# Kernel tuning notes

Measured on AMD Instinct MI355X. Metric: run time of the kernel, lower is better.

## Reference

```python
import jax, jax.numpy as jnp
import numpy as np

R = 65536          # N_rays
S = 128            # samples per ray
N = R * S          # total samples
L_OP = 0.05        # lambda_opacity (module arg)
L_DIST = 0.001     # lambda_distortion (module arg)
C_RGB = 1.0        # config.lambda_rgb
C_OP = 1.0         # config.lambda_opacity
C_EIK = 0.1        # config.lambda_eikonal


def setup_inputs() -> dict:
    key = jax.random.key(0)
    k = jax.random.split(key, 8)
    rgb = jax.random.uniform(k[0], (R, 3), dtype=jnp.float32)
    target_rays = jax.random.uniform(k[1], (R, 3), dtype=jnp.float32)
    opacity = jax.random.uniform(k[2], (R,), dtype=jnp.float32, minval=1e-4, maxval=1.0)
    grad = jax.random.normal(k[3], (N, 3), dtype=jnp.float32)
    ws = jax.random.uniform(k[4], (N,), dtype=jnp.float32) / S
    deltas = jax.random.uniform(k[5], (N,), dtype=jnp.float32) / S
    # midpoints sorted within each ray segment
    ts = jnp.sort(jax.random.uniform(k[6], (R, S), dtype=jnp.float32), axis=1).reshape(N)
    ray_idx = jax.random.permutation(k[7], R).astype(jnp.int32)
    rays_a = jnp.stack([ray_idx,
                        (jnp.arange(R) * S).astype(jnp.int32),
                        jnp.full((R,), S, dtype=jnp.int32)], axis=1)
    return dict(rgb=rgb, target_rays=target_rays, opacity=opacity, grad=grad,
                ws=ws, deltas=deltas, ts=ts, rays_a=rays_a)


def _smooth_l1(x, y):
    d = jnp.abs(x - y)
    return jnp.mean(jnp.where(d < 1.0, 0.5 * d * d, d - 0.5))


def _distortion_loss(ws, deltas, ts, rays_a):
    # Mip-NeRF 360 distortion via per-segment exclusive prefix sums:
    # loss_r = sum_i 2*w_i*(t_i*W_i^< - WT_i^<) + (1/3) sum_i w_i^2 * delta_i
    n = ws.shape[0]
    n_rays = rays_a.shape[0]
    ray_idx = rays_a[:, 0]
    starts = rays_a[:, 1]                      # sorted ascending (contiguous layout)
    pos = jnp.arange(n)
    seg = jnp.searchsorted(starts, pos, side='right') - 1   # row in rays_a per sample
    cw = jnp.cumsum(ws)
    cwt = jnp.cumsum(ws * ts)
    sm1 = jnp.maximum(starts - 1, 0)
    base_w = jnp.where(starts > 0, cw[sm1], 0.0)
    base_wt = jnp.where(starts > 0, cwt[sm1], 0.0)
    excl_w = cw - ws - base_w[seg]             # exclusive scan of w within segment
    excl_wt = cwt - ws * ts - base_wt[seg]     # exclusive scan of w*t within segment
    per = 2.0 * ws * (ts * excl_w - excl_wt) + ws * ws * deltas / 3.0
    per_row = jax.ops.segment_sum(per, seg, num_segments=n_rays)
    # scatter row losses to their ray index -> (N_rays,)
    return jnp.zeros(n_rays, ws.dtype).at[ray_idx].set(per_row)


def reference(rgb, target_rays, opacity, grad, ws, deltas, ts, rays_a):
    d_rgb = _smooth_l1(rgb, target_rays) * C_RGB
    d_op = L_OP * (-opacity * jnp.log(opacity)) * C_OP          # (N_rays,)
    d_eik = jnp.mean((jnp.linalg.norm(grad, axis=-1) - 1.0) ** 2) * C_EIK
    d_dist = L_DIST * _distortion_loss(ws, deltas, ts, rays_a)  # (N_rays,)
    # pack dict values into one flat array: [rgb, opacity(R), eikonal, distortion(R)]
    return jnp.concatenate([d_rgb[None], d_op, d_eik[None], d_dist])
```

## Files before the change

### kernel.cpp

```cpp
#include <hip/hip_runtime.h>
#include <math.h>

#define R_RAYS 65536
#define S_SAMP 128
#define NSLOTS 1024

__global__ void init_ws_kernel(float* __restrict__ w) {
    int i = blockIdx.x * blockDim.x + threadIdx.x;
    if (i < 2 * NSLOTS) w[i] = 0.f;
}

__device__ __forceinline__ float wave_incl_scan(float x, int lane) {
#pragma unroll
    for (int off = 1; off < 64; off <<= 1) {
        float v = __shfl_up(x, off, 64);
        if (lane >= off) x += v;
    }
    return x;
}

__global__ __launch_bounds__(128) void nerf_main_kernel(
    const float* __restrict__ rgb, const float* __restrict__ tgt,
    const float* __restrict__ opacity, const float* __restrict__ grad,
    const float* __restrict__ ws, const float* __restrict__ deltas,
    const float* __restrict__ ts, const int* __restrict__ rays_a,
    float* __restrict__ out, float* __restrict__ partials)
{
    const int r    = blockIdx.x;
    const int tid  = threadIdx.x;
    const int lane = tid & 63;
    const int wave = tid >> 6;

    const int ridx  = rays_a[3 * r + 0];
    const int start = rays_a[3 * r + 1];
    const int i = start + tid;

    const float w = ws[i];
    const float t = ts[i];
    const float d = deltas[i];
    const float wt = w * t;

    float iw  = wave_incl_scan(w, lane);
    float iwt = wave_incl_scan(wt, lane);
    __shared__ float s_w[2], s_wt[2];
    if (lane == 63) { s_w[wave] = iw; s_wt[wave] = iwt; }
    __syncthreads();
    const float bw  = (wave == 1) ? s_w[0]  : 0.f;
    const float bwt = (wave == 1) ? s_wt[0] : 0.f;
    const float ew  = iw  - w  + bw;
    const float ewt = iwt - wt + bwt;

    float per = 2.f * w * (t * ew - ewt) + w * w * d * (1.f / 3.f);

    const float gx = grad[3 * i + 0];
    const float gy = grad[3 * i + 1];
    const float gz = grad[3 * i + 2];
    const float nrm = sqrtf(gx * gx + gy * gy + gz * gz);
    float ek = (nrm - 1.f) * (nrm - 1.f);

#pragma unroll
    for (int off = 32; off > 0; off >>= 1) {
        per += __shfl_down(per, off, 64);
        ek  += __shfl_down(ek,  off, 64);
    }
    __shared__ float s_per[2], s_ek[2];
    if (lane == 0) { s_per[wave] = per; s_ek[wave] = ek; }
    __syncthreads();

    if (tid == 0) {
        out[2 + R_RAYS + ridx] = 0.001f * (s_per[0] + s_per[1]);
    } else if (tid == 1) {
        atomicAdd(&partials[r & (NSLOTS - 1)], s_ek[0] + s_ek[1]);
    } else if (tid == 2) {
        const float op = opacity[r];
        out[1 + r] = 0.05f * (-op * logf(op));
    } else if (tid == 3) {
        float srgb = 0.f;
#pragma unroll
        for (int c = 0; c < 3; ++c) {
            const float diff = fabsf(rgb[3 * r + c] - tgt[3 * r + c]);
            srgb += (diff < 1.f) ? 0.5f * diff * diff : (diff - 0.5f);
        }
        atomicAdd(&partials[NSLOTS + (r & (NSLOTS - 1))], srgb);
    }
}

__global__ __launch_bounds__(1024) void nerf_final_kernel(
    const float* __restrict__ partials, float* __restrict__ out)
{
    const int tid  = threadIdx.x;
    const int lane = tid & 63;
    const int wave = tid >> 6;

    float ek = partials[tid];
    float rg = partials[NSLOTS + tid];
#pragma unroll
    for (int off = 32; off > 0; off >>= 1) {
        ek += __shfl_down(ek, off, 64);
        rg += __shfl_down(rg, off, 64);
    }
    __shared__ float s_ek[16], s_rg[16];
    if (lane == 0) { s_ek[wave] = ek; s_rg[wave] = rg; }
    __syncthreads();
    if (tid == 0) {
        float tek = 0.f, trg = 0.f;
#pragma unroll
        for (int j = 0; j < 16; ++j) { tek += s_ek[j]; trg += s_rg[j]; }
        out[0]          = trg / (3.f * (float)R_RAYS);
        out[1 + R_RAYS] = 0.1f * tek / ((float)R_RAYS * (float)S_SAMP);
    }
}

extern "C" void kernel_launch(void* const* d_in, const int* in_sizes, int n_in,
                              void* d_out, int out_size, void* d_ws, size_t ws_size,
                              hipStream_t stream) {
    const float* rgb     = (const float*)d_in[0];
    const float* tgt     = (const float*)d_in[1];
    const float* opacity = (const float*)d_in[2];
    const float* grad    = (const float*)d_in[3];
    const float* ws      = (const float*)d_in[4];
    const float* deltas  = (const float*)d_in[5];
    const float* ts      = (const float*)d_in[6];
    const int*   rays_a  = (const int*)d_in[7];
    float* out      = (float*)d_out;
    float* partials = (float*)d_ws;

    init_ws_kernel<<<(2 * NSLOTS + 255) / 256, 256, 0, stream>>>(partials);
    nerf_main_kernel<<<R_RAYS, 128, 0, stream>>>(rgb, tgt, opacity, grad, ws,
                                                 deltas, ts, rays_a, out, partials);
    nerf_final_kernel<<<1, 1024, 0, stream>>>(partials, out);
}
```

Baseline: 238.9 us.

## Process 8 rays per block with float4 loads and per-block partials

Restructures the main kernel so each 32-lane group handles one ray with four samples per thread, loaded as float4, and does a thread-local serial scan followed by a 32-wide shuffle scan. The grid shrinks from 65536 blocks to 8192. The atomic accumulation into slots and the init kernel are replaced by deterministic per-block partial sums that the final kernel reduces. This cuts block-launch overhead, the wide scans and atomics, at the cost of more registers per thread and an assumption that segment starts are 16-byte aligned.

After: 230.6 us. 1.04x faster.

```diff
diff --git a/kernel.cpp b/kernel.cpp
--- a/kernel.cpp
+++ b/kernel.cpp
@@ -3,85 +3,103 @@
 
 #define R_RAYS 65536
 #define S_SAMP 128
-#define NSLOTS 1024
+#define RAYS_PER_BLOCK 8
+#define NB (R_RAYS / RAYS_PER_BLOCK)
 
-__global__ void init_ws_kernel(float* __restrict__ w) {
-    int i = blockIdx.x * blockDim.x + threadIdx.x;
-    if (i < 2 * NSLOTS) w[i] = 0.f;
-}
-
-__device__ __forceinline__ float wave_incl_scan(float x, int lane) {
-#pragma unroll
-    for (int off = 1; off < 64; off <<= 1) {
-        float v = __shfl_up(x, off, 64);
-        if (lane >= off) x += v;
-    }
-    return x;
-}
-
-__global__ __launch_bounds__(128) void nerf_main_kernel(
+__global__ __launch_bounds__(256) void nerf_main_kernel(
     const float* __restrict__ rgb, const float* __restrict__ tgt,
     const float* __restrict__ opacity, const float* __restrict__ grad,
     const float* __restrict__ ws, const float* __restrict__ deltas,
     const float* __restrict__ ts, const int* __restrict__ rays_a,
     float* __restrict__ out, float* __restrict__ partials)
 {
-    const int r    = blockIdx.x;
     const int tid  = threadIdx.x;
+    const int wave = tid >> 6;
     const int lane = tid & 63;
-    const int wave = tid >> 6;
+    const int grp  = tid >> 5;
+    const int l32  = tid & 31;
+    const int b    = blockIdx.x;
+    const int r    = b * RAYS_PER_BLOCK + grp;
 
     const int ridx  = rays_a[3 * r + 0];
     const int start = rays_a[3 * r + 1];
-    const int i = start + tid;
+    const int i0    = start + l32 * 4;
 
-    const float w = ws[i];
-    const float t = ts[i];
-    const float d = deltas[i];
-    const float wt = w * t;
+    const float4 w4 = *(const float4*)(ws + i0);
+    const float4 t4 = *(const float4*)(ts + i0);
+    const float4 d4 = *(const float4*)(deltas + i0);
+    const float wv[4] = { w4.x, w4.y, w4.z, w4.w };
+    const float tv[4] = { t4.x, t4.y, t4.z, t4.w };
+    const float dv[4] = { d4.x, d4.y, d4.z, d4.w };
 
-    float iw  = wave_incl_scan(w, lane);
-    float iwt = wave_incl_scan(wt, lane);
-    __shared__ float s_w[2], s_wt[2];
-    if (lane == 63) { s_w[wave] = iw; s_wt[wave] = iwt; }
-    __syncthreads();
-    const float bw  = (wave == 1) ? s_w[0]  : 0.f;
-    const float bwt = (wave == 1) ? s_wt[0] : 0.f;
-    const float ew  = iw  - w  + bw;
-    const float ewt = iwt - wt + bwt;
+    float wtv[4];
+    float sw = 0.f, swt = 0.f;
+#pragma unroll
+    for (int j = 0; j < 4; ++j) { wtv[j] = wv[j] * tv[j]; sw += wv[j]; swt += wtv[j]; }
 
-    float per = 2.f * w * (t * ew - ewt) + w * w * d * (1.f / 3.f);
+    float isw = sw, iswt = swt;
+#pragma unroll
+    for (int off = 1; off < 32; off <<= 1) {
+        const float a = __shfl_up(isw,  off, 32);
+        const float c = __shfl_up(iswt, off, 32);
+        if (l32 >= off) { isw += a; iswt += c; }
+    }
+    float ew  = isw  - sw;
+    float ewt = iswt - swt;
 
-    const float gx = grad[3 * i + 0];
-    const float gy = grad[3 * i + 1];
-    const float gz = grad[3 * i + 2];
-    const float nrm = sqrtf(gx * gx + gy * gy + gz * gz);
-    float ek = (nrm - 1.f) * (nrm - 1.f);
+    float per = 0.f;
+#pragma unroll
+    for (int j = 0; j < 4; ++j) {
+        per += 2.f * wv[j] * (tv[j] * ew - ewt) + wv[j] * wv[j] * dv[j] * (1.f / 3.f);
+        ew  += wv[j];
+        ewt += wtv[j];
+    }
+
+    const float* gp = grad + 3 * i0;
+    const float4 g0 = *(const float4*)(gp + 0);
+    const float4 g1 = *(const float4*)(gp + 4);
+    const float4 g2 = *(const float4*)(gp + 8);
+    float ek = 0.f;
+    {
+        float n;
+        n = sqrtf(g0.x*g0.x + g0.y*g0.y + g0.z*g0.z); ek += (n-1.f)*(n-1.f);
+        n = sqrtf(g0.w*g0.w + g1.x*g1.x + g1.y*g1.y); ek += (n-1.f)*(n-1.f);
+        n = sqrtf(g1.z*g1.z + g1.w*g1.w + g2.x*g2.x); ek += (n-1.f)*(n-1.f);
+        n = sqrtf(g2.y*g2.y + g2.z*g2.z + g2.w*g2.w); ek += (n-1.f)*(n-1.f);
+    }
 
 #pragma unroll
-    for (int off = 32; off > 0; off >>= 1) {
-        per += __shfl_down(per, off, 64);
-        ek  += __shfl_down(ek,  off, 64);
-    }
-    __shared__ float s_per[2], s_ek[2];
-    if (lane == 0) { s_per[wave] = per; s_ek[wave] = ek; }
-    __syncthreads();
+    for (int off = 16; off > 0; off >>= 1) per += __shfl_down(per, off, 32);
 
-    if (tid == 0) {
-        out[2 + R_RAYS + ridx] = 0.001f * (s_per[0] + s_per[1]);
-    } else if (tid == 1) {
-        atomicAdd(&partials[r & (NSLOTS - 1)], s_ek[0] + s_ek[1]);
-    } else if (tid == 2) {
+#pragma unroll
+    for (int off = 32; off > 0; off >>= 1) ek += __shfl_down(ek, off, 64);
+
+    __shared__ float s_ek[4], s_rg[8];
+    if (lane == 0) s_ek[wave] = ek;
+
+    if (l32 == 0) {
+        out[2 + R_RAYS + ridx] = 0.001f * per;
+    } else if (l32 == 1) {
         const float op = opacity[r];
         out[1 + r] = 0.05f * (-op * logf(op));
-    } else if (tid == 3) {
+    } else if (l32 == 2) {
         float srgb = 0.f;
 #pragma unroll
         for (int c = 0; c < 3; ++c) {
             const float diff = fabsf(rgb[3 * r + c] - tgt[3 * r + c]);
             srgb += (diff < 1.f) ? 0.5f * diff * diff : (diff - 0.5f);
         }
-        atomicAdd(&partials[NSLOTS + (r & (NSLOTS - 1))], srgb);
+        s_rg[grp] = srgb;
+    }
+    __syncthreads();
+
+    if (tid == 0) {
+        float bek = s_ek[0] + s_ek[1] + s_ek[2] + s_ek[3];
+        float brg = 0.f;
+#pragma unroll
+        for (int j = 0; j < 8; ++j) brg += s_rg[j];
+        partials[b]      = bek;
+        partials[NB + b] = brg;
     }
 }
 
@@ -92,8 +110,12 @@
     const int lane = tid & 63;
     const int wave = tid >> 6;
 
-    float ek = partials[tid];
-    float rg = partials[NSLOTS + tid];
+    float ek = 0.f, rg = 0.f;
+#pragma unroll
+    for (int k = 0; k < NB / 1024; ++k) {
+        ek += partials[tid + k * 1024];
+        rg += partials[NB + tid + k * 1024];
+    }
 #pragma unroll
     for (int off = 32; off > 0; off >>= 1) {
         ek += __shfl_down(ek, off, 64);
@@ -125,8 +147,7 @@
     float* out      = (float*)d_out;
     float* partials = (float*)d_ws;
 
-    init_ws_kernel<<<(2 * NSLOTS + 255) / 256, 256, 0, stream>>>(partials);
-    nerf_main_kernel<<<R_RAYS, 128, 0, stream>>>(rgb, tgt, opacity, grad, ws,
-                                                 deltas, ts, rays_a, out, partials);
+    nerf_main_kernel<<<NB, 256, 0, stream>>>(rgb, tgt, opacity, grad, ws,
+                                             deltas, ts, rays_a, out, partials);
     nerf_final_kernel<<<1, 1024, 0, stream>>>(partials, out);
 }
```
